# Optimization experiments

Hardware: AMD Instinct MI355X
Metric: run time of the kernel (lower is better)

## Reference

```python
import jax, jax.numpy as jnp
import numpy as np

D = 768

def _linear_params(key, name_idx, d_in, d_out):
    k1, k2 = jax.random.split(jax.random.fold_in(jax.random.key(42), name_idx))
    bound = 1.0 / np.sqrt(d_in)
    W = jax.random.uniform(k1, (d_out, d_in), jnp.float32, -bound, bound)
    b = jax.random.uniform(k2, (d_out,), jnp.float32, -bound, bound)
    return W, b

def setup_inputs() -> dict:
    key = jax.random.key(0)
    kq, kk, kv = jax.random.split(key, 3)
    B, S = 8, 2048
    inp = {
        'query': jax.random.normal(kq, (B, S, D), jnp.float32),
        'key': jax.random.normal(kk, (B, S, D), jnp.float32),
        'value': jax.random.normal(kv, (B, S, D), jnp.float32),
    }
    Wq, bq = _linear_params(key, 0, D, D)
    Wk, bk = _linear_params(key, 1, D, D)
    Wv, bv = _linear_params(key, 2, D, D)
    Wg1, bg1 = _linear_params(key, 3, D, D)
    Wg2, bg2 = _linear_params(key, 4, D, D)
    inp.update(Wq=Wq, bq=bq, Wk=Wk, bk=bk, Wv=Wv, bv=bv,
               Wg1=Wg1, bg1=bg1, Wg2=Wg2, bg2=bg2,
               text_scale=jnp.ones((1, D), jnp.float32))
    return inp

def reference(query, key, value, Wq, bq, Wk, bk, Wv, bv, Wg1, bg1, Wg2, bg2, text_scale):
    # Linear projections (torch Linear: x @ W.T + b)
    q = jnp.einsum('bsd,ed->bse', query, Wq) + bq
    k = jnp.einsum('bsd,ed->bse', key, Wk) + bk
    v = jnp.einsum('bsd,ed->bse', value, Wv) + bv
    scale = 1.0 / jnp.sqrt(jnp.float32(k.shape[-1]))
    scores = jnp.einsum('bqd,bkd->bqk', q, k) * scale  # [B, S, S]
    attn = jax.nn.softmax(scores, axis=-1)
    attended = jnp.einsum('bqk,bkd->bqd', attn, v)  # dropout = identity (eval)
    # text_gate: Linear -> ReLU -> Linear -> Sigmoid, then sigmoid applied AGAIN (faithful)
    h = jax.nn.relu(jnp.einsum('bsd,ed->bse', attended, Wg1) + bg1)
    gate = jax.nn.sigmoid(jnp.einsum('bsd,ed->bse', h, Wg2) + bg2)
    gated = jax.nn.sigmoid(gate) * attended * text_scale
    return gated
```

## Files before the change

### kernel.cpp

```cpp
#include <hip/hip_runtime.h>

typedef unsigned short ushort_t;
typedef __bf16 bf16x8 __attribute__((ext_vector_type(8)));
typedef float f32x4 __attribute__((ext_vector_type(4)));
typedef short short8 __attribute__((ext_vector_type(8)));

__device__ __forceinline__ float bf2f(unsigned short u) {
    union { unsigned int i; float f; } v; v.i = ((unsigned int)u) << 16; return v.f;
}
__device__ __forceinline__ unsigned short f2bf(float f) {
    union { float f; unsigned int i; } v; v.f = f;
    unsigned int r = v.i + 0x7fffu + ((v.i >> 16) & 1u);
    return (unsigned short)(r >> 16);
}
__device__ __forceinline__ float sigm(float x) { return 1.0f / (1.0f + __expf(-x)); }

__device__ __forceinline__ void async_copy16(const ushort_t* src, ushort_t* dst_lds) {
    __builtin_amdgcn_global_load_lds(
        (const __attribute__((address_space(1))) void*)src,
        (__attribute__((address_space(3))) void*)dst_lds,
        16, 0, 0);
}

#define WSEG 589824
#define NWALL 2949120
#define NTOT 2953728
__global__ __launch_bounds__(256)
void convert_params(const float* __restrict__ Wq, const float* __restrict__ Wk,
                    const float* __restrict__ Wv, const float* __restrict__ Wg1,
                    const float* __restrict__ Wg2, const float* __restrict__ bq,
                    const float* __restrict__ bk, const float* __restrict__ bv,
                    const float* __restrict__ bg1, const float* __restrict__ bg2,
                    const float* __restrict__ ts, ushort_t* __restrict__ dst)
{
    int i = (blockIdx.x * 256 + threadIdx.x) * 8;
    if (i >= NTOT) return;
    const float* src; int off;
    if (i < NWALL) {
        int wi = i / WSEG; off = i - wi * WSEG;
        src = (wi == 0) ? Wq : (wi == 1) ? Wk : (wi == 2) ? Wv : (wi == 3) ? Wg1 : Wg2;
    } else {
        int j = i - NWALL; int bi = j / 768; off = j - bi * 768;
        src = (bi == 0) ? bq : (bi == 1) ? bk : (bi == 2) ? bv : (bi == 3) ? bg1 : (bi == 4) ? bg2 : ts;
    }
    float4 a = *(const float4*)(src + off);
    float4 b = *(const float4*)(src + off + 4);
    short8 o;
    o[0] = (short)f2bf(a.x); o[1] = (short)f2bf(a.y); o[2] = (short)f2bf(a.z); o[3] = (short)f2bf(a.w);
    o[4] = (short)f2bf(b.x); o[5] = (short)f2bf(b.y); o[6] = (short)f2bf(b.z); o[7] = (short)f2bf(b.w);
    *(short8*)(dst + i) = o;
}

template<int EPI, int AF32, int CF32>
__global__ __launch_bounds__(256, 2)
void gemm_bt(const void* __restrict__ Av, const ushort_t* __restrict__ B,
             void* __restrict__ Cv, const ushort_t* __restrict__ bias,
             const ushort_t* __restrict__ aux, const ushort_t* __restrict__ ts,
             int M, int N, int K, float scale,
             long long batchA, long long batchB, long long batchC)
{
    __shared__ __align__(16) ushort_t As[128 * 32];
    __shared__ __align__(16) ushort_t Bs[128 * 32];
    const int tid  = threadIdx.x;
    const int lane = tid & 63;
    const int wave = tid >> 6;
    const int wr = wave >> 1, wc = wave & 1;

    const int gx = gridDim.x, gy = gridDim.y;
    const int nwg = gx * gy * gridDim.z;
    int fid = (blockIdx.z * gy + blockIdx.y) * gx + blockIdx.x;
    fid = (fid & 7) * (nwg >> 3) + (fid >> 3);
    const int bz  = fid / (gx * gy);
    const int rem = fid - bz * (gx * gy);
    const int by  = rem / gx;
    const int bx  = rem - by * gx;
    const int row0 = by * 128;
    const int col0 = bx * 128;

    f32x4 acc[4][4] = {};

    const int srow = tid >> 2;
    const int scol = (tid & 3) * 8;
    const ushort_t* ga0 = (const ushort_t*)Av + batchA * bz + (size_t)(row0 + srow) * K + scol;
    const ushort_t* gb0 = B + batchB * bz + (size_t)(col0 + srow) * K + scol;
    const int arow_s = tid >> 1;
    const int acol_s = (tid & 1) * 16;
    const float* gaf = (const float*)Av + batchA * bz + (size_t)(row0 + arow_s) * K + acol_s;

    const int kop  = (lane >> 4) * 8;
    const int arow = wr * 64 + (lane & 15);
    const int brow = wc * 64 + (lane & 15);

    for (int k0 = 0; k0 < K; k0 += 32) {
        if (AF32) {
            float4 fa0 = *(const float4*)(gaf + k0);
            float4 fa1 = *(const float4*)(gaf + k0 + 4);
            float4 fa2 = *(const float4*)(gaf + k0 + 8);
            float4 fa3 = *(const float4*)(gaf + k0 + 12);
            async_copy16(gb0 + k0,                  Bs + tid * 8);
            async_copy16(gb0 + (size_t)64 * K + k0, Bs + 2048 + tid * 8);
            short8 p0, p1;
            p0[0] = (short)f2bf(fa0.x); p0[1] = (short)f2bf(fa0.y);
            p0[2] = (short)f2bf(fa0.z); p0[3] = (short)f2bf(fa0.w);
            p0[4] = (short)f2bf(fa1.x); p0[5] = (short)f2bf(fa1.y);
            p0[6] = (short)f2bf(fa1.z); p0[7] = (short)f2bf(fa1.w);
            p1[0] = (short)f2bf(fa2.x); p1[1] = (short)f2bf(fa2.y);
            p1[2] = (short)f2bf(fa2.z); p1[3] = (short)f2bf(fa2.w);
            p1[4] = (short)f2bf(fa3.x); p1[5] = (short)f2bf(fa3.y);
            p1[6] = (short)f2bf(fa3.z); p1[7] = (short)f2bf(fa3.w);
            *(short8*)(As + arow_s * 32 + acol_s)     = p0;
            *(short8*)(As + arow_s * 32 + acol_s + 8) = p1;
        } else {
            async_copy16(ga0 + k0,                  As + tid * 8);
            async_copy16(ga0 + (size_t)64 * K + k0, As + 2048 + tid * 8);
            async_copy16(gb0 + k0,                  Bs + tid * 8);
            async_copy16(gb0 + (size_t)64 * K + k0, Bs + 2048 + tid * 8);
        }
        asm volatile("s_waitcnt vmcnt(0)" ::: "memory");
        __syncthreads();

        bf16x8 af[4], bfr[4];
        #pragma unroll
        for (int m = 0; m < 4; ++m)
            af[m] = *(const bf16x8*)(As + (arow + m * 16) * 32 + kop);
        #pragma unroll
        for (int n = 0; n < 4; ++n)
            bfr[n] = *(const bf16x8*)(Bs + (brow + n * 16) * 32 + kop);
        #pragma unroll
        for (int m = 0; m < 4; ++m)
            #pragma unroll
            for (int n = 0; n < 4; ++n)
                acc[m][n] = __builtin_amdgcn_mfma_f32_16x16x32_bf16(af[m], bfr[n], acc[m][n], 0, 0, 0);
        __syncthreads();
    }

    const int r0 = row0 + wr * 64 + (lane >> 4) * 4;
    const int c0 = col0 + wc * 64 + (lane & 15);
    #pragma unroll
    for (int m = 0; m < 4; ++m) {
        #pragma unroll
        for (int n = 0; n < 4; ++n) {
            const int col = c0 + n * 16;
            #pragma unroll
            for (int r = 0; r < 4; ++r) {
                const int row = r0 + m * 16 + r;
                float val = acc[m][n][r];
                if (EPI == 1) {
                    val += bf2f(bias[col]);
                } else if (EPI == 2) {
                    val *= scale;
                } else if (EPI == 3) {
                    val += bf2f(bias[col]);
                    val = fmaxf(val, 0.0f);
                } else if (EPI == 4) {
                    val += bf2f(bias[col]);
                    float g  = sigm(val);
                    float gg = sigm(g);
                    val = gg * bf2f(aux[(size_t)row * N + col]) * bf2f(ts[col]);
                }
                if (CF32) ((float*)Cv)[batchC * bz + (size_t)row * N + col] = val;
                else      ((ushort_t*)Cv)[batchC * bz + (size_t)row * N + col] = f2bf(val);
            }
        }
    }
}

__global__ __launch_bounds__(256)
void softmax_inplace(ushort_t* __restrict__ P, int S)
{
    const size_t row = blockIdx.x;
    ushort_t* p = P + row * (size_t)S;
    const int tid = threadIdx.x;
    const int lane = tid & 63, wave = tid >> 6;

    short8 raw = *(const short8*)(p + tid * 8);
    float x[8];
    #pragma unroll
    for (int j = 0; j < 8; ++j) x[j] = bf2f((unsigned short)raw[j]);

    float mx = x[0];
    #pragma unroll
    for (int j = 1; j < 8; ++j) mx = fmaxf(mx, x[j]);
    #pragma unroll
    for (int o = 32; o > 0; o >>= 1) mx = fmaxf(mx, __shfl_xor(mx, o));
    __shared__ float redm[4], reds[4];
    if (lane == 0) redm[wave] = mx;
    __syncthreads();
    mx = fmaxf(fmaxf(redm[0], redm[1]), fmaxf(redm[2], redm[3]));

    float s = 0.f;
    #pragma unroll
    for (int j = 0; j < 8; ++j) { x[j] = __expf(x[j] - mx); s += x[j]; }
    #pragma unroll
    for (int o = 32; o > 0; o >>= 1) s += __shfl_xor(s, o);
    if (lane == 0) reds[wave] = s;
    __syncthreads();
    s = reds[0] + reds[1] + reds[2] + reds[3];
    const float inv = 1.0f / s;

    short8 outv;
    #pragma unroll
    for (int j = 0; j < 8; ++j) outv[j] = (short)f2bf(x[j] * inv);
    *(short8*)(p + tid * 8) = outv;
}

__global__ __launch_bounds__(256)
void transpose2d(const ushort_t* __restrict__ V, ushort_t* __restrict__ VT, int R, int Ccols)
{
    __shared__ ushort_t t[32][33];
    const size_t zoff = (size_t)blockIdx.z * R * Ccols;
    const int tx = threadIdx.x, ty = threadIdx.y;
    const int c = blockIdx.x * 32 + tx;
    const int rbase = blockIdx.y * 32;
    #pragma unroll
    for (int i = 0; i < 4; ++i)
        t[ty + i * 8][tx] = V[zoff + (size_t)(rbase + ty + i * 8) * Ccols + c];
    __syncthreads();
    const int r = rbase + tx;
    const int cbase = blockIdx.x * 32;
    #pragma unroll
    for (int i = 0; i < 4; ++i)
        VT[zoff + (size_t)(cbase + ty + i * 8) * R + r] = t[tx][ty + i * 8];
}

extern "C" void kernel_launch(void* const* d_in, const int* in_sizes, int n_in,
                              void* d_out, int out_size, void* d_ws, size_t ws_size,
                              hipStream_t stream)
{
    (void)in_sizes; (void)n_in; (void)out_size;
    const float* query = (const float*)d_in[0];
    const float* key_  = (const float*)d_in[1];
    const float* value = (const float*)d_in[2];
    const float* Wq  = (const float*)d_in[3];
    const float* bq  = (const float*)d_in[4];
    const float* Wk  = (const float*)d_in[5];
    const float* bk  = (const float*)d_in[6];
    const float* Wv  = (const float*)d_in[7];
    const float* bv  = (const float*)d_in[8];
    const float* Wg1 = (const float*)d_in[9];
    const float* bg1 = (const float*)d_in[10];
    const float* Wg2 = (const float*)d_in[11];
    const float* bg2 = (const float*)d_in[12];
    const float* tsc = (const float*)d_in[13];

    const int S = 2048, D = 768, Bc = 8;
    const int MS = Bc * S;
    const long long SD = (long long)S * D;
    const long long SS = (long long)S * S;

    char* ws = (char*)d_ws;
    ushort_t* q   = (ushort_t*)(ws);
    ushort_t* att = q;
    ushort_t* k   = (ushort_t*)(ws + 25165824ll);
    ushort_t* h   = k;
    ushort_t* vT  = (ushort_t*)(ws + 50331648ll);
    ushort_t* Wb  = (ushort_t*)(ws + 75497472ll);
    ushort_t* P   = (ushort_t*)(ws + 81404928ll);
    ushort_t* v   = (ushort_t*)d_out;

    const int WQ = 0, WK = 589824, WV = 1179648, WG1 = 1769472, WG2 = 2359296;
    const int BQ = 2949120, BK = 2949888, BV = 2950656, BG1 = 2951424, BG2 = 2952192, TSO = 2952960;

    const dim3 blk(256);
    const float scale = 0.03608439182435161f;
    const bool batched = ws_size >= 148513792ull;

    convert_params<<<dim3((NTOT / 8 + 255) / 256), blk, 0, stream>>>(
        Wq, Wk, Wv, Wg1, Wg2, bq, bk, bv, bg1, bg2, tsc, Wb);
    gemm_bt<1, 1, 0><<<dim3(D / 128, MS / 128), blk, 0, stream>>>(query, Wb + WQ, q, Wb + BQ, nullptr, nullptr, MS, D, D, 1.f, 0, 0, 0);
    gemm_bt<1, 1, 0><<<dim3(D / 128, MS / 128), blk, 0, stream>>>(key_,  Wb + WK, k, Wb + BK, nullptr, nullptr, MS, D, D, 1.f, 0, 0, 0);
    gemm_bt<1, 1, 0><<<dim3(D / 128, MS / 128), blk, 0, stream>>>(value, Wb + WV, v, Wb + BV, nullptr, nullptr, MS, D, D, 1.f, 0, 0, 0);
    transpose2d<<<dim3(D / 32, S / 32, Bc), dim3(32, 8), 0, stream>>>(v, vT, S, D);
    if (batched) {
        gemm_bt<2, 0, 0><<<dim3(S / 128, S / 128, Bc), blk, 0, stream>>>(q, k, P, nullptr, nullptr, nullptr, S, S, D, scale, SD, SD, SS);
        softmax_inplace<<<dim3(MS), blk, 0, stream>>>(P, S);
        gemm_bt<0, 0, 0><<<dim3(D / 128, S / 128, Bc), blk, 0, stream>>>(P, vT, att, nullptr, nullptr, nullptr, S, D, S, 1.f, SS, SD, SD);
    } else {
        for (int z = 0; z < Bc; ++z) {
            gemm_bt<2, 0, 0><<<dim3(S / 128, S / 128), blk, 0, stream>>>(q + (size_t)z * SD, k + (size_t)z * SD, P,
                                                                          nullptr, nullptr, nullptr, S, S, D, scale, 0, 0, 0);
            softmax_inplace<<<dim3(S), blk, 0, stream>>>(P, S);
            gemm_bt<0, 0, 0><<<dim3(D / 128, S / 128), blk, 0, stream>>>(P, vT + (size_t)z * SD, att + (size_t)z * SD,
                                                                          nullptr, nullptr, nullptr, S, D, S, 1.f, 0, 0, 0);
        }
    }
    gemm_bt<3, 0, 0><<<dim3(D / 128, MS / 128), blk, 0, stream>>>(att, Wb + WG1, h, Wb + BG1, nullptr, nullptr, MS, D, D, 1.f, 0, 0, 0);
    gemm_bt<4, 0, 1><<<dim3(D / 128, MS / 128), blk, 0, stream>>>(h, Wb + WG2, d_out, Wb + BG2, att, Wb + TSO, MS, D, D, 1.f, 0, 0, 0);
}
```

Measured before the change: 374.7 us.

## Double-buffer GEMM shared-memory tiles to overlap global loads with MFMA

Converts the GEMM main loop to double-buffered LDS tiles. The next K-slice is prefetched with async global-to-LDS copies, or register loads on the fp32 path, while MFMAs run on the current slice, using explicit vmcnt waits and raw s_barrier. This aims to hide global memory latency that previously stalled every iteration on vmcnt(0). It doubles LDS use per block to 32KB, which may affect occupancy. It also adds a batch offset to the aux read in the gating epilogue.

```diff
diff --git a/kernel.cpp b/kernel.cpp
--- a/kernel.cpp
+++ b/kernel.cpp
@@ -4,6 +4,13 @@
 typedef __bf16 bf16x8 __attribute__((ext_vector_type(8)));
 typedef float f32x4 __attribute__((ext_vector_type(4)));
 typedef short short8 __attribute__((ext_vector_type(8)));
+
+#define SBAR()   asm volatile("s_barrier" ::: "memory")
+#define WAITV0() asm volatile("s_waitcnt vmcnt(0)" ::: "memory")
+#define WAITV2() asm volatile("s_waitcnt vmcnt(2)" ::: "memory")
+#define WAITV4() asm volatile("s_waitcnt vmcnt(4)" ::: "memory")
+#define WAITV6() asm volatile("s_waitcnt vmcnt(6)" ::: "memory")
+#define WAITL0() asm volatile("s_waitcnt lgkmcnt(0)" ::: "memory")
 
 __device__ __forceinline__ float bf2f(unsigned short u) {
     union { unsigned int i; float f; } v; v.i = ((unsigned int)u) << 16; return v.f;
@@ -59,8 +66,8 @@
              int M, int N, int K, float scale,
              long long batchA, long long batchB, long long batchC)
 {
-    __shared__ __align__(16) ushort_t As[128 * 32];
-    __shared__ __align__(16) ushort_t Bs[128 * 32];
+    __shared__ __align__(16) ushort_t As[2][128 * 32];
+    __shared__ __align__(16) ushort_t Bs[2][128 * 32];
     const int tid  = threadIdx.x;
     const int lane = tid & 63;
     const int wave = tid >> 6;
@@ -91,14 +98,19 @@
     const int arow = wr * 64 + (lane & 15);
     const int brow = wc * 64 + (lane & 15);
 
-    for (int k0 = 0; k0 < K; k0 += 32) {
-        if (AF32) {
-            float4 fa0 = *(const float4*)(gaf + k0);
-            float4 fa1 = *(const float4*)(gaf + k0 + 4);
-            float4 fa2 = *(const float4*)(gaf + k0 + 8);
-            float4 fa3 = *(const float4*)(gaf + k0 + 12);
-            async_copy16(gb0 + k0,                  Bs + tid * 8);
-            async_copy16(gb0 + (size_t)64 * K + k0, Bs + 2048 + tid * 8);
+    const int NT = K >> 5;
+
+    if (AF32) {
+        float4 fa0 = *(const float4*)(gaf);
+        float4 fa1 = *(const float4*)(gaf + 4);
+        float4 fa2 = *(const float4*)(gaf + 8);
+        float4 fa3 = *(const float4*)(gaf + 12);
+        async_copy16(gb0,                  Bs[0] + tid * 8);
+        async_copy16(gb0 + (size_t)64 * K, Bs[0] + 2048 + tid * 8);
+
+        for (int t = 0; t < NT; ++t) {
+            const int cur = t & 1;
+            WAITV2();
             short8 p0, p1;
             p0[0] = (short)f2bf(fa0.x); p0[1] = (short)f2bf(fa0.y);
             p0[2] = (short)f2bf(fa0.z); p0[3] = (short)f2bf(fa0.w);
@@ -108,30 +120,69 @@
             p1[2] = (short)f2bf(fa2.z); p1[3] = (short)f2bf(fa2.w);
             p1[4] = (short)f2bf(fa3.x); p1[5] = (short)f2bf(fa3.y);
             p1[6] = (short)f2bf(fa3.z); p1[7] = (short)f2bf(fa3.w);
-            *(short8*)(As + arow_s * 32 + acol_s)     = p0;
-            *(short8*)(As + arow_s * 32 + acol_s + 8) = p1;
-        } else {
-            async_copy16(ga0 + k0,                  As + tid * 8);
-            async_copy16(ga0 + (size_t)64 * K + k0, As + 2048 + tid * 8);
-            async_copy16(gb0 + k0,                  Bs + tid * 8);
-            async_copy16(gb0 + (size_t)64 * K + k0, Bs + 2048 + tid * 8);
+            *(short8*)(As[cur] + arow_s * 32 + acol_s)     = p0;
+            *(short8*)(As[cur] + arow_s * 32 + acol_s + 8) = p1;
+            if (t + 1 < NT) {
+                const int k1 = (t + 1) * 32;
+                fa0 = *(const float4*)(gaf + k1);
+                fa1 = *(const float4*)(gaf + k1 + 4);
+                fa2 = *(const float4*)(gaf + k1 + 8);
+                fa3 = *(const float4*)(gaf + k1 + 12);
+                async_copy16(gb0 + k1,                  Bs[cur ^ 1] + tid * 8);
+                async_copy16(gb0 + (size_t)64 * K + k1, Bs[cur ^ 1] + 2048 + tid * 8);
+                WAITV6();
+            } else {
+                WAITV0();
+            }
+            WAITL0();
+            SBAR();
+            bf16x8 af[4], bfr[4];
+            #pragma unroll
+            for (int m = 0; m < 4; ++m)
+                af[m] = *(const bf16x8*)(As[cur] + (arow + m * 16) * 32 + kop);
+            #pragma unroll
+            for (int n = 0; n < 4; ++n)
+                bfr[n] = *(const bf16x8*)(Bs[cur] + (brow + n * 16) * 32 + kop);
+            #pragma unroll
+            for (int m = 0; m < 4; ++m)
+                #pragma unroll
+                for (int n = 0; n < 4; ++n)
+                    acc[m][n] = __builtin_amdgcn_mfma_f32_16x16x32_bf16(af[m], bfr[n], acc[m][n], 0, 0, 0);
+            SBAR();
         }
-        asm volatile("s_waitcnt vmcnt(0)" ::: "memory");
-        __syncthreads();
-
-        bf16x8 af[4], bfr[4];
-        #pragma unroll
-        for (int m = 0; m < 4; ++m)
-            af[m] = *(const bf16x8*)(As + (arow + m * 16) * 32 + kop);
-        #pragma unroll
-        for (int n = 0; n < 4; ++n)
-            bfr[n] = *(const bf16x8*)(Bs + (brow + n * 16) * 32 + kop);
-        #pragma unroll
-        for (int m = 0; m < 4; ++m)
+    } else {
+        async_copy16(ga0,                  As[0] + tid * 8);
+        async_copy16(ga0 + (size_t)64 * K, As[0] + 2048 + tid * 8);
+        async_copy16(gb0,                  Bs[0] + tid * 8);
+        async_copy16(gb0 + (size_t)64 * K, Bs[0] + 2048 + tid * 8);
+
+        for (int t = 0; t < NT; ++t) {
+            const int cur = t & 1;
+            if (t + 1 < NT) {
+                const int k1 = (t + 1) * 32;
+                async_copy16(ga0 + k1,                  As[cur ^ 1] + tid * 8);
+                async_copy16(ga0 + (size_t)64 * K + k1, As[cur ^ 1] + 2048 + tid * 8);
+                async_copy16(gb0 + k1,                  Bs[cur ^ 1] + tid * 8);
+                async_copy16(gb0 + (size_t)64 * K + k1, Bs[cur ^ 1] + 2048 + tid * 8);
+                WAITV4();
+            } else {
+                WAITV0();
+            }
+            SBAR();
+            bf16x8 af[4], bfr[4];
+            #pragma unroll
+            for (int m = 0; m < 4; ++m)
+                af[m] = *(const bf16x8*)(As[cur] + (arow + m * 16) * 32 + kop);
             #pragma unroll
             for (int n = 0; n < 4; ++n)
-                acc[m][n] = __builtin_amdgcn_mfma_f32_16x16x32_bf16(af[m], bfr[n], acc[m][n], 0, 0, 0);
-        __syncthreads();
+                bfr[n] = *(const bf16x8*)(Bs[cur] + (brow + n * 16) * 32 + kop);
+            #pragma unroll
+            for (int m = 0; m < 4; ++m)
+                #pragma unroll
+                for (int n = 0; n < 4; ++n)
+                    acc[m][n] = __builtin_amdgcn_mfma_f32_16x16x32_bf16(af[m], bfr[n], acc[m][n], 0, 0, 0);
+            SBAR();
+        }
     }
 
     const int r0 = row0 + wr * 64 + (lane >> 4) * 4;
@@ -156,7 +207,7 @@
                     val += bf2f(bias[col]);
                     float g  = sigm(val);
                     float gg = sigm(g);
-                    val = gg * bf2f(aux[(size_t)row * N + col]) * bf2f(ts[col]);
+                    val = gg * bf2f(aux[batchC * bz + (size_t)row * N + col]) * bf2f(ts[col]);
                 }
                 if (CF32) ((float*)Cv)[batchC * bz + (size_t)row * N + col] = val;
                 else      ((ushort_t*)Cv)[batchC * bz + (size_t)row * N + col] = f2bf(val);
```

Measured after the change: 374.1 us. About the same (-0.1%).
